# Optimization experiments

Measured on AMD Instinct MI355X. Metric: run time of the kernel, lower is better.

The kernel has to match this reference:

```python
import jax, jax.numpy as jnp
import numpy as np
import math

N_HEAD = 8
LN_EPS = 1e-5


def _layernorm(x, g, b):
    mu = jnp.mean(x, axis=-1, keepdims=True)
    var = jnp.mean(jnp.square(x - mu), axis=-1, keepdims=True)
    return (x - mu) / jnp.sqrt(var + LN_EPS) * g + b


def setup_inputs() -> dict:
    key0 = jax.random.key(0)
    ks = jax.random.split(key0, 12)
    B, L, D, E = 4, 512, 256, 5  # batch, agents, n_embd, edge_feats_dim

    def w(k, shape):
        return jax.random.normal(k, shape, dtype=jnp.float32) * 0.02

    return {
        "key": jax.random.normal(ks[0], (B, L, D), jnp.float32),
        "value": jax.random.normal(ks[1], (B, L, D), jnp.float32),
        "query": jax.random.normal(ks[2], (B, L, D), jnp.float32),
        "atten_masks": jax.random.randint(ks[3], (B, L, L), 0, 2).astype(jnp.int32),
        "edge_feats": jax.random.normal(ks[4], (B, L, L, E), jnp.float32),
        # Linear weights stored [in, out] so forward is x @ W + b
        "Wk": w(ks[5], (D, D)), "bk": jnp.zeros((D,), jnp.float32),
        "Wq": w(ks[6], (D, D)), "bq": jnp.zeros((D,), jnp.float32),
        "Wv": w(ks[7], (D, D)), "bv": jnp.zeros((D,), jnp.float32),
        "Wp": w(ks[8], (D, D)), "bp": jnp.zeros((D,), jnp.float32),
        "We1": w(ks[9], (E, D)), "be1": jnp.zeros((D,), jnp.float32),
        "ln_g": jnp.ones((D,), jnp.float32), "ln_b": jnp.zeros((D,), jnp.float32),
        "We2": w(ks[10], (D, N_HEAD)), "be2": jnp.zeros((N_HEAD,), jnp.float32),
    }


def reference(key, value, query, atten_masks, edge_feats,
              Wk, bk, Wq, bq, Wv, bv, Wp, bp,
              We1, be1, ln_g, ln_b, We2, be2):
    B, L, D = query.shape
    hd = D // N_HEAD
    # QKV projections -> [B, H, L, hd]
    q = (query @ Wq + bq).reshape(B, L, N_HEAD, hd).transpose(0, 2, 1, 3)
    k = (key @ Wk + bk).reshape(B, L, N_HEAD, hd).transpose(0, 2, 1, 3)
    v = (value @ Wv + bv).reshape(B, L, N_HEAD, hd).transpose(0, 2, 1, 3)
    # scaled attention scores [B, H, L, L]
    att = jnp.einsum('bhqd,bhkd->bhqk', q, k) * (1.0 / math.sqrt(hd))
    # edge-feature additive bias: Linear -> ReLU -> LayerNorm -> Linear(per-head)
    e = jax.nn.relu(edge_feats @ We1 + be1)          # [B, L, L, D]
    e = _layernorm(e, ln_g, ln_b)
    e = e @ We2 + be2                                # [B, L, L, H]
    att = att + e.transpose(0, 3, 1, 2)
    # additive mask (0 -> -inf), softmax over keys
    att = jnp.where(atten_masks[:, None, :, :] == 0, -jnp.inf, att)
    att = jax.nn.softmax(att, axis=-1)
    y = jnp.einsum('bhqk,bhkd->bhqd', att, v)        # [B, H, L, hd]
    y = y.transpose(0, 2, 1, 3).reshape(B, L, D)
    return y @ Wp + bp
```

## Files before the change

kernel.cpp:

```cpp
#include <hip/hip_runtime.h>
#include <hip/hip_bf16.h>

#define L_SEQ 512
#define D_EMB 256
#define NH 8
#define HD 32
#define LL (L_SEQ * L_SEQ)

typedef __attribute__((ext_vector_type(8))) short short8;
typedef __attribute__((ext_vector_type(4))) float f32x4;
typedef unsigned short ushort;

__device__ __forceinline__ float bf2f(ushort u) {
    unsigned int x = ((unsigned int)u) << 16;
    float f;
    __builtin_memcpy(&f, &x, 4);
    return f;
}
__device__ __forceinline__ ushort f2bf(float x) {
    __hip_bfloat16 h = __float2bfloat16(x);
    ushort u;
    __builtin_memcpy(&u, &h, 2);
    return u;
}
__device__ __forceinline__ unsigned int fbits(float x) {
    unsigned int u;
    __builtin_memcpy(&u, &x, 4);
    return u;
}
__device__ __forceinline__ float asf(unsigned int u) {
    float f;
    __builtin_memcpy(&f, &u, 4);
    return f;
}
__device__ __forceinline__ unsigned int pack_bf16rnd(float a, float b) {
    return __builtin_amdgcn_perm(fbits(b) + 0x8000u, fbits(a) + 0x8000u, 0x07060302u);
}
__device__ __forceinline__ unsigned int packhi(unsigned int y, unsigned int x) {
    return __builtin_amdgcn_perm(y, x, 0x07060302u);
}
__device__ __forceinline__ uint2 cvt_hilo2(float v0, float v1) {
    unsigned int hi = pack_bf16rnd(v0, v1);
    float h0 = asf(hi << 16);
    float h1 = asf(hi & 0xffff0000u);
    unsigned int lo = pack_bf16rnd(v0 - h0, v1 - h1);
    uint2 r; r.x = hi; r.y = lo;
    return r;
}

__global__ __launch_bounds__(256) void prep_kernel(
    const float* __restrict__ We1, const float* __restrict__ be1,
    const float* __restrict__ g,   const float* __restrict__ bta,
    const float* __restrict__ We2, const float* __restrict__ be2,
    const float* __restrict__ Wq, const float* __restrict__ Wk,
    const float* __restrict__ Wv, const float* __restrict__ Wp,
    ushort* __restrict__ W1G, ushort* __restrict__ B2G, float* __restrict__ tail,
    ushort* __restrict__ WThi, ushort* __restrict__ WTlo)
{
    int t = threadIdx.x;
    if (blockIdx.x != 0) {
        int bx = blockIdx.x - 1;
        int w = bx >> 4, ny = bx & 15;
        const float* W = (w == 0) ? Wq : (w == 1) ? Wk : (w == 2) ? Wv : Wp;
        ushort* dh = WThi + (size_t)w * 65536;
        ushort* dl = WTlo + (size_t)w * 65536;
        int n = ny * 16 + (t >> 4);
        int k0 = (t & 15) * 16;
        ushort hbuf[16], lbuf[16];
#pragma unroll
        for (int kk = 0; kk < 16; ++kk) {
            float v = W[(size_t)(k0 + kk) * 256 + n];
            unsigned int hb = fbits(v) + 0x8000u;
            ushort hi = (ushort)(hb >> 16);
            float res = v - bf2f(hi);
            hbuf[kk] = hi;
            lbuf[kk] = (ushort)((fbits(res) + 0x8000u) >> 16);
        }
        *(short8*)(dh + (size_t)n * 256 + k0)     = *(short8*)&hbuf[0];
        *(short8*)(dh + (size_t)n * 256 + k0 + 8) = *(short8*)&hbuf[8];
        *(short8*)(dl + (size_t)n * 256 + k0)     = *(short8*)&lbuf[0];
        *(short8*)(dl + (size_t)n * 256 + k0 + 8) = *(short8*)&lbuf[8];
        return;
    }

    __shared__ float red[16][256];
    float gd = g[t], bd = bta[t];
#pragma unroll
    for (int h = 0; h < 8; ++h) {
        float w2 = We2[t * 8 + h];
        red[h][t] = gd * w2;
        red[8 + h][t] = bd * w2;
    }
    __syncthreads();
    for (int off = 128; off > 0; off >>= 1) {
        if (t < off) {
#pragma unroll
            for (int row = 0; row < 16; ++row) red[row][t] += red[row][t + off];
        }
        __syncthreads();
    }
    if (t < 8) {
        tail[t] = red[t][0];
        tail[8 + t] = red[8 + t][0] + be2[t];
    }
    if (t >= 16 && t < 32) tail[t] = 0.f;

    for (int idx = t; idx < 8192; idx += 256) {
        int j = idx & 7, lane = (idx >> 3) & 63, tile = idx >> 9;
        int m = lane & 15, q = lane >> 4;
        int k = q * 8 + j;
        int d = (m >> 2) * 64 + tile * 4 + (m & 3);
        float v = 0.f;
        bool lo = false;
        if (k < 5)        v = We1[k * 256 + d];
        else if (k < 10)  { v = We1[(k - 5) * 256 + d]; lo = true; }
        else if (k < 15)  v = We1[(k - 10) * 256 + d];
        else if (k == 15) v = be1[d];
        else if (k == 16) { v = be1[d]; lo = true; }
        ushort hi = f2bf(v);
        W1G[idx] = lo ? f2bf(v - bf2f(hi)) : hi;
    }
    for (int idx = t; idx < 4096; idx += 256) {
        int j = idx & 7, lane = (idx >> 3) & 63, kc = idx >> 9;
        int n = lane & 15, q = lane >> 4;
        int d = kc * 32 + q * 8 + j;
        ushort out;
        if (n < 8)       out = f2bf(g[d] * We2[d * 8 + n]);
        else if (n == 8) out = 0x3F80;
        else             out = 0;
        B2G[idx] = out;
    }
}

__device__ __forceinline__ void gemm_body(
    const float* __restrict__ A, const ushort* __restrict__ BH,
    const ushort* __restrict__ BL, const float* __restrict__ bias,
    float* __restrict__ C, float* __restrict__ Ct,
    int bx, int by, char* smem)
{
    ushort* Ahi = (ushort*)smem;
    ushort* Alo = (ushort*)(smem + 5120);

    int tid = threadIdx.x;
    int wv = tid >> 6, lane = tid & 63;
    int m = lane & 15, quad = lane >> 4;
    int bm = bx * 64, bn = by * 64;

    int sm = tid >> 2, sg = (tid & 3) * 8;
    const float* Arow = A + (size_t)(bm + sm) * 256 + sg;

    int nrow = bn + wv * 16 + m;
    const ushort* bhp = BH + (size_t)nrow * 256 + quad * 8;
    const ushort* blp = BL + (size_t)nrow * 256 + quad * 8;

    f32x4 acc[4];
#pragma unroll
    for (int mt = 0; mt < 4; ++mt) acc[mt] = (f32x4){0.f, 0.f, 0.f, 0.f};

    for (int k0 = 0; k0 < 256; k0 += 32) {
        float4 a0 = *(const float4*)(Arow + k0);
        float4 a1 = *(const float4*)(Arow + k0 + 4);
        uint2 c0 = cvt_hilo2(a0.x, a0.y);
        uint2 c1 = cvt_hilo2(a0.z, a0.w);
        uint2 c2 = cvt_hilo2(a1.x, a1.y);
        uint2 c3 = cvt_hilo2(a1.z, a1.w);
        if (k0) __syncthreads();
        uint4 hq; hq.x = c0.x; hq.y = c1.x; hq.z = c2.x; hq.w = c3.x;
        uint4 lq; lq.x = c0.y; lq.y = c1.y; lq.z = c2.y; lq.w = c3.y;
        *(uint4*)&Ahi[sm * 40 + sg] = hq;
        *(uint4*)&Alo[sm * 40 + sg] = lq;
        __syncthreads();

        short8 bhi = *(const short8*)(bhp + k0);
        short8 blo = *(const short8*)(blp + k0);
#pragma unroll
        for (int mt = 0; mt < 4; ++mt) {
            short8 ahi = *(const short8*)&Ahi[(mt * 16 + m) * 40 + quad * 8];
            short8 alo = *(const short8*)&Alo[(mt * 16 + m) * 40 + quad * 8];
            acc[mt] = __builtin_amdgcn_mfma_f32_16x16x32_bf16(ahi, blo, acc[mt], 0, 0, 0);
            acc[mt] = __builtin_amdgcn_mfma_f32_16x16x32_bf16(alo, bhi, acc[mt], 0, 0, 0);
            acc[mt] = __builtin_amdgcn_mfma_f32_16x16x32_bf16(ahi, bhi, acc[mt], 0, 0, 0);
        }
    }

    float bn_bias = bias[nrow];
    if (Ct) {
        int bb = bm >> 9, l0 = bm & 511;
        float* outp = Ct + ((size_t)(bb * 256 + nrow)) * 512 + l0 + quad * 4;
#pragma unroll
        for (int mt = 0; mt < 4; ++mt) {
            float4 o;
            o.x = acc[mt][0] + bn_bias; o.y = acc[mt][1] + bn_bias;
            o.z = acc[mt][2] + bn_bias; o.w = acc[mt][3] + bn_bias;
            *(float4*)(outp + mt * 16) = o;
        }
    } else {
#pragma unroll
        for (int mt = 0; mt < 4; ++mt) {
#pragma unroll
            for (int r = 0; r < 4; ++r) {
                C[(size_t)(bm + mt * 16 + quad * 4 + r) * 256 + nrow] = acc[mt][r] + bn_bias;
            }
        }
    }
}

__device__ __forceinline__ void edge_body(
    const float* __restrict__ EF, const ushort* __restrict__ W1G,
    const ushort* __restrict__ B2G, const float* __restrict__ tail,
    ushort* __restrict__ E2, int bi, char* smem)
{
    int tid = threadIdx.x;
    int wv = tid >> 6, lane = tid & 63;
    int q = lane >> 4, n = lane & 15;
    char* myx = smem + wv * (16 * 528);

    int b = bi >> 9, i = bi & 511;
    size_t rowbase = (size_t)bi * 512;

    short8 w1f[16];
#pragma unroll
    for (int t = 0; t < 16; ++t)
        w1f[t] = *(const short8*)(W1G + (t * 64 + lane) * 8);
    short8 b2f[8];
#pragma unroll
    for (int kc = 0; kc < 8; ++kc)
        b2f[kc] = *(const short8*)(B2G + (kc * 64 + lane) * 8);

    float shv = tail[n];
    float bbv = tail[8 + n];
    const float inv256 = 1.0f / 256.0f;

    const float* efbase = EF + rowbase * 5;
    int pairoff = wv * 16 + n;

    float4 evA = *(const float4*)(efbase + (size_t)pairoff * 5);
    float  evB = efbase[(size_t)pairoff * 5 + 4];

    for (int iter = 0; iter < 8; ++iter) {
        float4 nA; float nB;
        if (iter < 7) {
            const float* p = efbase + (size_t)((iter + 1) * 64 + pairoff) * 5;
            nA = *(const float4*)p;
            nB = p[4];
        }
        int jb = iter * 64 + wv * 16;

        unsigned int hb[5], la[5];
        hb[0] = fbits(evA.x); hb[1] = fbits(evA.y); hb[2] = fbits(evA.z);
        hb[3] = fbits(evA.w); hb[4] = fbits(evB);
        {
            float e0 = evA.x - asf(hb[0] & 0xffff0000u);
            float e1 = evA.y - asf(hb[1] & 0xffff0000u);
            float e2 = evA.z - asf(hb[2] & 0xffff0000u);
            float e3 = evA.w - asf(hb[3] & 0xffff0000u);
            float e4 = evB   - asf(hb[4] & 0xffff0000u);
            la[0] = fbits(e0) + 0x8000u;
            la[1] = fbits(e1) + 0x8000u;
            la[2] = fbits(e2) + 0x8000u;
            la[3] = fbits(e3) + 0x8000u;
            la[4] = fbits(e4) + 0x8000u;
        }
        unsigned int A0v = packhi(hb[1], hb[0]);
        unsigned int A1v = packhi(hb[3], hb[2]);
        unsigned int A2v = packhi(hb[0], hb[4]);
        unsigned int A3v = packhi(hb[2], hb[1]);
        unsigned int B0v = packhi(hb[4], hb[3]);
        unsigned int B1v = packhi(la[1], la[0]);
        unsigned int B2v = packhi(la[3], la[2]);
        unsigned int B3v = packhi(0x3F800000u, la[4]);
        uint4 efd;
        bool isq0 = (q == 0), isq1 = (q == 1), isq2 = (q == 2);
        efd.x = isq0 ? A0v : isq1 ? B0v : isq2 ? 0x3F80u : 0u;
        efd.y = isq0 ? A1v : isq1 ? B1v : 0u;
        efd.z = isq0 ? A2v : isq1 ? B2v : 0u;
        efd.w = isq0 ? A3v : isq1 ? B3v : 0u;
        short8 ef8;
        __builtin_memcpy(&ef8, &efd, 16);

        unsigned int pk0 = 0, pk1 = 0;
#pragma unroll
        for (int t = 0; t < 16; ++t) {
            f32x4 z = {0.f, 0.f, 0.f, 0.f};
            f32x4 d1 = __builtin_amdgcn_mfma_f32_16x16x32_bf16(w1f[t], ef8, z, 0, 0, 0);
            float x0 = fmaxf(d1[0], 0.f);
            float x1 = fmaxf(d1[1], 0.f);
            float x2 = fmaxf(d1[2], 0.f);
            float x3 = fmaxf(d1[3], 0.f);
            unsigned int pa = pack_bf16rnd(x0, x1);
            unsigned int pb = pack_bf16rnd(x2, x3);
            if (t & 1) {
                uint4 wq; wq.x = pk0; wq.y = pk1; wq.z = pa; wq.w = pb;
                *(uint4*)(myx + n * 528 + q * 128 + (t - 1) * 8) = wq;
            } else {
                pk0 = pa; pk1 = pb;
            }
        }

        f32x4 acc  = {0.f, 0.f, 0.f, 0.f};
        f32x4 acc2 = {0.f, 0.f, 0.f, 0.f};
#pragma unroll
        for (int kc = 0; kc < 8; ++kc) {
            short8 a = *(const short8*)(myx + n * 528 + kc * 64 + q * 16);
            acc  = __builtin_amdgcn_mfma_f32_16x16x32_bf16(a, b2f[kc], acc, 0, 0, 0);
            acc2 = __builtin_amdgcn_mfma_f32_16x16x32_bf16(a, a, acc2, 0, 0, 0);
        }

        int base = lane & 48;
        float er[4];
#pragma unroll
        for (int r = 0; r < 4; ++r) {
            float sm = __shfl(acc[r], base + 8);
            float sq = __shfl(acc2[r], base + (base >> 2) + r);
            float dot = acc[r];
            float mu = sm * inv256;
            float var = fmaf(-mu, mu, sq * inv256);
            float rs = rsqrtf(var + 1e-5f);
            er[r] = fmaf(dot - mu * shv, rs, bbv);
        }
        if (n < 8) {
            uint2 outv;
            outv.x = pack_bf16rnd(er[0], er[1]);
            outv.y = pack_bf16rnd(er[2], er[3]);
            size_t basep = (((size_t)(b * NH + n) * L_SEQ + i) * L_SEQ) + jb + q * 4;
            *(uint2*)(E2 + basep) = outv;
        }
        evA = nA; evB = nB;
    }
}

__global__ __launch_bounds__(256) void fused_qkv_edge(
    const float* __restrict__ query, const float* __restrict__ key,
    const float* __restrict__ value,
    const ushort* __restrict__ WThi, const ushort* __restrict__ WTlo,
    const float* __restrict__ bq, const float* __restrict__ bk,
    const float* __restrict__ bv,
    float* __restrict__ Qw, float* __restrict__ Ktw, float* __restrict__ Vw,
    const float* __restrict__ EF, const ushort* __restrict__ W1G,
    const ushort* __restrict__ B2G, const float* __restrict__ tail,
    ushort* __restrict__ E2)
{
    __shared__ __align__(16) char smem[4 * 16 * 528];
    int bid = blockIdx.x;
    if (bid < 384) {
        int z = bid >> 7, rem = bid & 127;
        int bx = rem & 31, by = rem >> 5;
        if (z == 0)
            gemm_body(query, WThi + 0 * 65536, WTlo + 0 * 65536, bq, Qw, nullptr, bx, by, smem);
        else if (z == 1)
            gemm_body(key,   WThi + 1 * 65536, WTlo + 1 * 65536, bk, nullptr, Ktw, bx, by, smem);
        else
            gemm_body(value, WThi + 2 * 65536, WTlo + 2 * 65536, bv, Vw, nullptr, bx, by, smem);
    } else {
        edge_body(EF, W1G, B2G, tail, E2, bid - 384, smem);
    }
}

__global__ __launch_bounds__(256) void gemm_out(
    const float* __restrict__ A, const ushort* __restrict__ BH,
    const ushort* __restrict__ BL, const float* __restrict__ bias,
    float* __restrict__ C)
{
    __shared__ __align__(16) char smem[10240];
    gemm_body(A, BH, BL, bias, C, nullptr, blockIdx.x, blockIdx.y, smem);
}

__global__ __launch_bounds__(256, 4) void attn_kernel(
    const float* __restrict__ Q, const float* __restrict__ Kt,
    const float* __restrict__ V, const ushort* __restrict__ E2,
    const int* __restrict__ MSK, float* __restrict__ Y)
{
    __shared__ float stage[4096];
    __shared__ ushort pbuf[4][512][4];

    int bh = blockIdx.x;
    int b = bh >> 3, h = bh & 7;
    int tid = threadIdx.x;
    int wv = tid >> 6, lane = tid & 63;
    int i0 = blockIdx.y * 16;
    int i = i0 + wv * 4;

    const float* Ktb = Kt + (size_t)bh * (HD * L_SEQ);
    const float* Vb  = V + (size_t)b * L_SEQ * D_EMB + h * HD;

    int wvu = __builtin_amdgcn_readfirstlane(wv);
    const float* Qs = Q + ((size_t)(b * L_SEQ + i0 + wvu * 4)) * 256 + h * HD;

    size_t erow = ((size_t)bh * L_SEQ + i) * L_SEQ;
    size_t mrow = ((size_t)b * L_SEQ + i) * L_SEQ;

    unsigned int e2p[4][4];
    int2 mkp[4][4];
#pragma unroll
    for (int r = 0; r < 4; ++r)
#pragma unroll
        for (int c = 0; c < 4; ++c) {
            int j = c * 128 + 2 * lane;
            e2p[r][c] = *(const unsigned int*)(E2 + erow + (size_t)r * L_SEQ + j);
            mkp[r][c] = *(const int2*)(MSK + mrow + (size_t)r * L_SEQ + j);
        }

    float s[4][8];
#pragma unroll
    for (int r = 0; r < 4; ++r)
#pragma unroll
        for (int t = 0; t < 8; ++t) s[r][t] = 0.f;

    for (int c = 0; c < 4; ++c) {
        if (c) __syncthreads();
        {
            int d0 = tid >> 5, jj = (tid & 31) * 4;
#pragma unroll
            for (int p = 0; p < 4; ++p) {
                int d = p * 8 + d0;
                float4 kv = *(const float4*)(Ktb + (size_t)d * L_SEQ + c * 128 + jj);
                *(float4*)&stage[d * 128 + jj] = kv;
            }
        }
        __syncthreads();
        int c2 = c * 2;
#pragma unroll
        for (int d = 0; d < HD; ++d) {
            float q0 = Qs[0 * 256 + d];
            float q1 = Qs[1 * 256 + d];
            float q2 = Qs[2 * 256 + d];
            float q3 = Qs[3 * 256 + d];
            float2 kv = *(const float2*)&stage[d * 128 + 2 * lane];
            s[0][c2]     = fmaf(q0, kv.x, s[0][c2]);
            s[0][c2 + 1] = fmaf(q0, kv.y, s[0][c2 + 1]);
            s[1][c2]     = fmaf(q1, kv.x, s[1][c2]);
            s[1][c2 + 1] = fmaf(q1, kv.y, s[1][c2 + 1]);
            s[2][c2]     = fmaf(q2, kv.x, s[2][c2]);
            s[2][c2 + 1] = fmaf(q2, kv.y, s[2][c2 + 1]);
            s[3][c2]     = fmaf(q3, kv.x, s[3][c2]);
            s[3][c2 + 1] = fmaf(q3, kv.y, s[3][c2 + 1]);
        }
    }

    const float scl = 0.17677669529663687f;
#pragma unroll
    for (int r = 0; r < 4; ++r) {
        float m = -3.0e38f;
#pragma unroll
        for (int idx = 0; idx < 8; ++idx) {
            int c = idx >> 1, u = idx & 1;
            unsigned int pk = e2p[r][c];
            float e = bf2f((ushort)(u ? (pk >> 16) : (pk & 0xffff)));
            int mk = u ? mkp[r][c].y : mkp[r][c].x;
            float v = (mk != 0) ? fmaf(s[r][idx], scl, e) : -1e30f;
            s[r][idx] = v;
            m = fmaxf(m, v);
        }
#pragma unroll
        for (int o = 32; o > 0; o >>= 1) m = fmaxf(m, __shfl_xor(m, o));
        float ssum = 0.f;
#pragma unroll
        for (int idx = 0; idx < 8; ++idx) {
            float p = __expf(s[r][idx] - m);
            s[r][idx] = p;
            ssum += p;
        }
#pragma unroll
        for (int o = 32; o > 0; o >>= 1) ssum += __shfl_xor(ssum, o);
        float inv = 1.0f / ssum;
#pragma unroll
        for (int idx = 0; idx < 8; ++idx) s[r][idx] *= inv;
    }
#pragma unroll
    for (int c = 0; c < 4; ++c) {
        int c2 = c * 2;
        uint4 w;
        w.x = pack_bf16rnd(s[0][c2],     s[1][c2]);
        w.y = pack_bf16rnd(s[2][c2],     s[3][c2]);
        w.z = pack_bf16rnd(s[0][c2 + 1], s[1][c2 + 1]);
        w.w = pack_bf16rnd(s[2][c2 + 1], s[3][c2 + 1]);
        *(uint4*)&pbuf[wv][c * 128 + 2 * lane][0] = w;
    }

    int dg = lane >> 3, js = lane & 7;
    float4 acc[4];
#pragma unroll
    for (int r = 0; r < 4; ++r) { acc[r].x = 0.f; acc[r].y = 0.f; acc[r].z = 0.f; acc[r].w = 0.f; }

    for (int c = 0; c < 4; ++c) {
        __syncthreads();
        {
            int j0 = tid >> 3, dd = (tid & 7) * 4;
#pragma unroll
            for (int p = 0; p < 4; ++p) {
                int j = p * 32 + j0;
                float4 vv = *(const float4*)(Vb + (size_t)(c * 128 + j) * D_EMB + dd);
                *(float4*)&stage[j * 32 + dd] = vv;
            }
        }
        __syncthreads();
#pragma unroll
        for (int jb = 0; jb < 16; ++jb) {
            int jj = jb * 8 + js;
            float4 v4 = *(const float4*)&stage[jj * 32 + dg * 4];
            uint2 pu = *(const uint2*)&pbuf[wv][c * 128 + jj][0];
            float p0 = asf(pu.x << 16);
            float p1 = asf(pu.x & 0xffff0000u);
            float p2 = asf(pu.y << 16);
            float p3 = asf(pu.y & 0xffff0000u);
            acc[0].x = fmaf(p0, v4.x, acc[0].x);
            acc[0].y = fmaf(p0, v4.y, acc[0].y);
            acc[0].z = fmaf(p0, v4.z, acc[0].z);
            acc[0].w = fmaf(p0, v4.w, acc[0].w);
            acc[1].x = fmaf(p1, v4.x, acc[1].x);
            acc[1].y = fmaf(p1, v4.y, acc[1].y);
            acc[1].z = fmaf(p1, v4.z, acc[1].z);
            acc[1].w = fmaf(p1, v4.w, acc[1].w);
            acc[2].x = fmaf(p2, v4.x, acc[2].x);
            acc[2].y = fmaf(p2, v4.y, acc[2].y);
            acc[2].z = fmaf(p2, v4.z, acc[2].z);
            acc[2].w = fmaf(p2, v4.w, acc[2].w);
            acc[3].x = fmaf(p3, v4.x, acc[3].x);
            acc[3].y = fmaf(p3, v4.y, acc[3].y);
            acc[3].z = fmaf(p3, v4.z, acc[3].z);
            acc[3].w = fmaf(p3, v4.w, acc[3].w);
        }
    }

#pragma unroll
    for (int off = 1; off < 8; off <<= 1) {
#pragma unroll
        for (int r = 0; r < 4; ++r) {
            acc[r].x += __shfl_xor(acc[r].x, off);
            acc[r].y += __shfl_xor(acc[r].y, off);
            acc[r].z += __shfl_xor(acc[r].z, off);
            acc[r].w += __shfl_xor(acc[r].w, off);
        }
    }
    if (js == 0) {
#pragma unroll
        for (int r = 0; r < 4; ++r)
            *(float4*)(Y + ((size_t)(b * L_SEQ + i + r)) * 256 + h * HD + dg * 4) = acc[r];
    }
}

extern "C" void kernel_launch(void* const* d_in, const int* in_sizes, int n_in,
                              void* d_out, int out_size, void* d_ws, size_t ws_size,
                              hipStream_t stream)
{
    const float* key   = (const float*)d_in[0];
    const float* value = (const float*)d_in[1];
    const float* query = (const float*)d_in[2];
    const int*   msk   = (const int*)d_in[3];
    const float* ef    = (const float*)d_in[4];
    const float* Wk  = (const float*)d_in[5];  const float* bk  = (const float*)d_in[6];
    const float* Wq  = (const float*)d_in[7];  const float* bq  = (const float*)d_in[8];
    const float* Wv  = (const float*)d_in[9];  const float* bv  = (const float*)d_in[10];
    const float* Wp  = (const float*)d_in[11]; const float* bp  = (const float*)d_in[12];
    const float* We1 = (const float*)d_in[13]; const float* be1 = (const float*)d_in[14];
    const float* lng = (const float*)d_in[15]; const float* lnb = (const float*)d_in[16];
    const float* We2 = (const float*)d_in[17]; const float* be2 = (const float*)d_in[18];

    const int MTOK = 4 * L_SEQ;
    const int NELT = MTOK * D_EMB;

    float* ws    = (float*)d_ws;
    float* Qw    = ws;
    float* Vw    = Qw + NELT;
    float* Yw    = Vw + NELT;
    float* Ktw   = Yw + NELT;
    ushort* W1G  = (ushort*)(Ktw + NELT);
    ushort* B2G  = W1G + 8192;
    float* tail  = (float*)(B2G + 4096);
    ushort* WThi = (ushort*)(tail + 32);
    ushort* WTlo = WThi + 4 * 65536;
    ushort* E2   = WTlo + 4 * 65536;

    hipLaunchKernelGGL(prep_kernel, dim3(65), dim3(256), 0, stream,
                       We1, be1, lng, lnb, We2, be2,
                       Wq, Wk, Wv, Wp,
                       W1G, B2G, tail, WThi, WTlo);
    hipLaunchKernelGGL(fused_qkv_edge, dim3(2432), dim3(256), 0, stream,
                       query, key, value, WThi, WTlo, bq, bk, bv,
                       Qw, Ktw, Vw,
                       ef, W1G, B2G, tail, E2);
    hipLaunchKernelGGL(attn_kernel, dim3(32, 32), dim3(256), 0, stream,
                       Qw, Ktw, Vw, E2, msk, Yw);
    hipLaunchKernelGGL(gemm_out, dim3(32, 4), dim3(256), 0, stream,
                       Yw, WThi + 3 * 65536, WTlo + 3 * 65536, bp, (float*)d_out);
}
```

Before: 220.6 us.

## Chain edge MLP MFMAs in registers and use hardware bf16 pack conversion

The edge-bias path no longer writes the ReLU'd first-layer activations to LDS and reads them back. It permutes the B2G weight layout so that each pair of first-layer MFMA outputs lines up directly as an A operand for the second-layer and sum-of-squares MFMAs. Two independent accumulator chains are alternated to hide MFMA latency. The manual add-and-permute bf16 packing is replaced by the v_cvt_pk_bf16_f32 instruction everywhere, which changes rounding slightly to round-to-nearest-even, and the fused kernel's shared memory allocation shrinks.

```diff
diff --git a/kernel.cpp b/kernel.cpp
--- a/kernel.cpp
+++ b/kernel.cpp
@@ -33,17 +33,19 @@
     __builtin_memcpy(&f, &u, 4);
     return f;
 }
-__device__ __forceinline__ unsigned int pack_bf16rnd(float a, float b) {
-    return __builtin_amdgcn_perm(fbits(b) + 0x8000u, fbits(a) + 0x8000u, 0x07060302u);
+__device__ __forceinline__ unsigned int cvt_pk_bf16(float a, float b) {
+    unsigned int r;
+    asm("v_cvt_pk_bf16_f32 %0, %1, %2" : "=v"(r) : "v"(a), "v"(b));
+    return r;
 }
 __device__ __forceinline__ unsigned int packhi(unsigned int y, unsigned int x) {
     return __builtin_amdgcn_perm(y, x, 0x07060302u);
 }
 __device__ __forceinline__ uint2 cvt_hilo2(float v0, float v1) {
-    unsigned int hi = pack_bf16rnd(v0, v1);
+    unsigned int hi = cvt_pk_bf16(v0, v1);
     float h0 = asf(hi << 16);
     float h1 = asf(hi & 0xffff0000u);
-    unsigned int lo = pack_bf16rnd(v0 - h0, v1 - h1);
+    unsigned int lo = cvt_pk_bf16(v0 - h0, v1 - h1);
     uint2 r; r.x = hi; r.y = lo;
     return r;
 }
@@ -123,7 +125,7 @@
     for (int idx = t; idx < 4096; idx += 256) {
         int j = idx & 7, lane = (idx >> 3) & 63, kc = idx >> 9;
         int n = lane & 15, q = lane >> 4;
-        int d = kc * 32 + q * 8 + j;
+        int d = q * 64 + kc * 8 + j;
         ushort out;
         if (n < 8)       out = f2bf(g[d] * We2[d * 8 + n]);
         else if (n == 8) out = 0x3F80;
@@ -208,12 +210,11 @@
 __device__ __forceinline__ void edge_body(
     const float* __restrict__ EF, const ushort* __restrict__ W1G,
     const ushort* __restrict__ B2G, const float* __restrict__ tail,
-    ushort* __restrict__ E2, int bi, char* smem)
+    ushort* __restrict__ E2, int bi)
 {
     int tid = threadIdx.x;
     int wv = tid >> 6, lane = tid & 63;
     int q = lane >> 4, n = lane & 15;
-    char* myx = smem + wv * (16 * 528);
 
     int b = bi >> 9, i = bi & 511;
     size_t rowbase = (size_t)bi * 512;
@@ -278,33 +279,30 @@
         short8 ef8;
         __builtin_memcpy(&ef8, &efd, 16);
 
-        unsigned int pk0 = 0, pk1 = 0;
-#pragma unroll
-        for (int t = 0; t < 16; ++t) {
-            f32x4 z = {0.f, 0.f, 0.f, 0.f};
-            f32x4 d1 = __builtin_amdgcn_mfma_f32_16x16x32_bf16(w1f[t], ef8, z, 0, 0, 0);
-            float x0 = fmaxf(d1[0], 0.f);
-            float x1 = fmaxf(d1[1], 0.f);
-            float x2 = fmaxf(d1[2], 0.f);
-            float x3 = fmaxf(d1[3], 0.f);
-            unsigned int pa = pack_bf16rnd(x0, x1);
-            unsigned int pb = pack_bf16rnd(x2, x3);
-            if (t & 1) {
-                uint4 wq; wq.x = pk0; wq.y = pk1; wq.z = pa; wq.w = pb;
-                *(uint4*)(myx + n * 528 + q * 128 + (t - 1) * 8) = wq;
+        const f32x4 z = {0.f, 0.f, 0.f, 0.f};
+        f32x4 acc  = z, acc2  = z;
+        f32x4 accB = z, acc2B = z;
+#pragma unroll
+        for (int kc = 0; kc < 8; ++kc) {
+            f32x4 dA = __builtin_amdgcn_mfma_f32_16x16x32_bf16(w1f[2 * kc],     ef8, z, 0, 0, 0);
+            f32x4 dB = __builtin_amdgcn_mfma_f32_16x16x32_bf16(w1f[2 * kc + 1], ef8, z, 0, 0, 0);
+            uint4 av;
+            av.x = cvt_pk_bf16(fmaxf(dA[0], 0.f), fmaxf(dA[1], 0.f));
+            av.y = cvt_pk_bf16(fmaxf(dA[2], 0.f), fmaxf(dA[3], 0.f));
+            av.z = cvt_pk_bf16(fmaxf(dB[0], 0.f), fmaxf(dB[1], 0.f));
+            av.w = cvt_pk_bf16(fmaxf(dB[2], 0.f), fmaxf(dB[3], 0.f));
+            short8 a;
+            __builtin_memcpy(&a, &av, 16);
+            if (kc & 1) {
+                accB  = __builtin_amdgcn_mfma_f32_16x16x32_bf16(a, b2f[kc], accB, 0, 0, 0);
+                acc2B = __builtin_amdgcn_mfma_f32_16x16x32_bf16(a, a,       acc2B, 0, 0, 0);
             } else {
-                pk0 = pa; pk1 = pb;
+                acc  = __builtin_amdgcn_mfma_f32_16x16x32_bf16(a, b2f[kc], acc, 0, 0, 0);
+                acc2 = __builtin_amdgcn_mfma_f32_16x16x32_bf16(a, a,       acc2, 0, 0, 0);
             }
         }
-
-        f32x4 acc  = {0.f, 0.f, 0.f, 0.f};
-        f32x4 acc2 = {0.f, 0.f, 0.f, 0.f};
-#pragma unroll
-        for (int kc = 0; kc < 8; ++kc) {
-            short8 a = *(const short8*)(myx + n * 528 + kc * 64 + q * 16);
-            acc  = __builtin_amdgcn_mfma_f32_16x16x32_bf16(a, b2f[kc], acc, 0, 0, 0);
-            acc2 = __builtin_amdgcn_mfma_f32_16x16x32_bf16(a, a, acc2, 0, 0, 0);
-        }
+        acc  = acc + accB;
+        acc2 = acc2 + acc2B;
 
         int base = lane & 48;
         float er[4];
@@ -320,8 +318,8 @@
         }
         if (n < 8) {
             uint2 outv;
-            outv.x = pack_bf16rnd(er[0], er[1]);
-            outv.y = pack_bf16rnd(er[2], er[3]);
+            outv.x = cvt_pk_bf16(er[0], er[1]);
+            outv.y = cvt_pk_bf16(er[2], er[3]);
             size_t basep = (((size_t)(b * NH + n) * L_SEQ + i) * L_SEQ) + jb + q * 4;
             *(uint2*)(E2 + basep) = outv;
         }
@@ -340,7 +338,7 @@
     const ushort* __restrict__ B2G, const float* __restrict__ tail,
     ushort* __restrict__ E2)
 {
-    __shared__ __align__(16) char smem[4 * 16 * 528];
+    __shared__ __align__(16) char smem[10240];
     int bid = blockIdx.x;
     if (bid < 384) {
         int z = bid >> 7, rem = bid & 127;
@@ -352,7 +350,7 @@
         else
             gemm_body(value, WThi + 2 * 65536, WTlo + 2 * 65536, bv, Vw, nullptr, bx, by, smem);
     } else {
-        edge_body(EF, W1G, B2G, tail, E2, bid - 384, smem);
+        edge_body(EF, W1G, B2G, tail, E2, bid - 384);
     }
 }
 
@@ -470,10 +468,10 @@
     for (int c = 0; c < 4; ++c) {
         int c2 = c * 2;
         uint4 w;
-        w.x = pack_bf16rnd(s[0][c2],     s[1][c2]);
-        w.y = pack_bf16rnd(s[2][c2],     s[3][c2]);
-        w.z = pack_bf16rnd(s[0][c2 + 1], s[1][c2 + 1]);
-        w.w = pack_bf16rnd(s[2][c2 + 1], s[3][c2 + 1]);
+        w.x = cvt_pk_bf16(s[0][c2],     s[1][c2]);
+        w.y = cvt_pk_bf16(s[2][c2],     s[3][c2]);
+        w.z = cvt_pk_bf16(s[0][c2 + 1], s[1][c2 + 1]);
+        w.w = cvt_pk_bf16(s[2][c2 + 1], s[3][c2 + 1]);
         *(uint4*)&pbuf[wv][c * 128 + 2 * lane][0] = w;
     }
 
```

Result: faster. 212.5 us (-3.7%).
